# Optimization experiments

Hardware: AMD Instinct MI355X
Metric: run time of the kernel (lower is better)

The kernel has to match this reference:

```python
import jax, jax.numpy as jnp
import numpy as np
import math

B, D, OUT, K = 128, 128, 100000, 4096
T = 0.07
# NOTE: original code reads momentum as params[4], which is -1 (params = [K, T, -1, -1, -1, momentum]).
# We replicate this faithfully: effective momentum = -1.0.
MOMENTUM = -1.0


def setup_inputs() -> dict:
    key = jax.random.key(0)
    k1, k2, k3, k4, k5, k6, k7 = jax.random.split(key, 7)
    stdv = 1.0 / math.sqrt(D / 3)
    return {
        "z1": jax.random.normal(k1, (B, D), dtype=jnp.float32),
        "z2": jax.random.normal(k2, (B, D), dtype=jnp.float32),
        "z3": jax.random.normal(k3, (B, D), dtype=jnp.float32),
        "memory_z2": jax.random.uniform(k4, (OUT, D), dtype=jnp.float32, minval=-stdv, maxval=stdv),
        "memory_z3": jax.random.uniform(k5, (OUT, D), dtype=jnp.float32, minval=-stdv, maxval=stdv),
        "y": jax.random.randint(k6, (B,), 0, OUT, dtype=jnp.int32),
        "idx": jax.random.randint(k7, (B, K + 1), 0, OUT, dtype=jnp.int32),
    }


def _scores(memory, idx, z1, outputSize):
    # gather [B, K+1, D] rows, per-row dot with z1 -> [B, K+1]
    w = jax.lax.stop_gradient(memory)[idx]
    s = jnp.exp(jnp.einsum('bkd,bd->bk', w, z1) / T)[..., None]  # [B, K+1, 1]
    Z = jax.lax.stop_gradient(jnp.mean(s) * outputSize)  # Z_* set on first call
    return s / Z


def _update(memory, y, z):
    pos = memory[y] * MOMENTUM + z * (1.0 - MOMENTUM)  # [B, D]
    pos = pos / jnp.sqrt(jnp.sum(pos * pos, axis=1, keepdims=True))
    return memory.at[y].set(pos)


def reference(z1, z2, z3, memory_z2, memory_z3, y, idx):
    outputSize = memory_z2.shape[0]
    # mimic idx=None path: first column of idx is the positive index y
    idx = idx.at[:, 0].set(y)
    I_z12 = _scores(memory_z2, idx, z1, outputSize)
    I_z13 = _scores(memory_z3, idx, z1, outputSize)
    new_mem2 = _update(memory_z2, y, z2)
    new_mem3 = _update(memory_z3, y, z3)
    return (I_z12, I_z13, new_mem2, new_mem3)
```

## Files before the change

### kernel.cpp

```cpp
#include <hip/hip_runtime.h>

#define BB   128
#define DD   128
#define OUTN 100000
#define KP1  4097
#define TEMP 0.07f

#define NSB   8320
#define N1F4  3200000
#define NF4   6400000
#define CSTRIDE (NSB * 256)
#define SCORES (2 * BB * KP1)
#define NSCALE_BLK 4097

typedef float vfloat4 __attribute__((ext_vector_type(4)));

__global__ __launch_bounds__(256) void fused_kernel(
    const float* __restrict__ z1,
    const float* __restrict__ mem2,
    const float* __restrict__ mem3,
    const int*   __restrict__ y,
    const int*   __restrict__ idx,
    float* __restrict__ out,
    float* __restrict__ part)
{
    const int sb    = blockIdx.x;
    const int b     = sb & (BB - 1);
    const int chunk = sb >> 7;
    const int tid   = threadIdx.x;
    const int g     = tid & 7;
    const int grp   = tid >> 3;

    const float4* zz = (const float4*)(z1 + (size_t)b * DD + g * 16);
    const float4 z0 = zz[0], zv1 = zz[1], zv2 = zz[2], zv3 = zz[3];

    const int yb = y[b];

    float acc2 = 0.f, acc3 = 0.f;

    for (int it = 0; it < 2; ++it) {
        const int k = chunk * 64 + it * 32 + grp;
        const bool valid = (k < KP1);
        int j = 0;
        if (valid) j = (k == 0) ? yb : idx[b * KP1 + k];

        const float4* r2 = (const float4*)(mem2 + (size_t)j * DD + g * 16);
        const float4* r3 = (const float4*)(mem3 + (size_t)j * DD + g * 16);
        const float4 a0 = r2[0], a1 = r2[1], a2 = r2[2], a3 = r2[3];
        const float4 c0 = r3[0], c1 = r3[1], c2 = r3[2], c3 = r3[3];

        float d2 = a0.x*z0.x  + a0.y*z0.y  + a0.z*z0.z  + a0.w*z0.w
                 + a1.x*zv1.x + a1.y*zv1.y + a1.z*zv1.z + a1.w*zv1.w
                 + a2.x*zv2.x + a2.y*zv2.y + a2.z*zv2.z + a2.w*zv2.w
                 + a3.x*zv3.x + a3.y*zv3.y + a3.z*zv3.z + a3.w*zv3.w;
        float d3 = c0.x*z0.x  + c0.y*z0.y  + c0.z*z0.z  + c0.w*z0.w
                 + c1.x*zv1.x + c1.y*zv1.y + c1.z*zv1.z + c1.w*zv1.w
                 + c2.x*zv2.x + c2.y*zv2.y + c2.z*zv2.z + c2.w*zv2.w
                 + c3.x*zv3.x + c3.y*zv3.y + c3.z*zv3.z + c3.w*zv3.w;

        d2 += __shfl_xor(d2, 1);  d3 += __shfl_xor(d3, 1);
        d2 += __shfl_xor(d2, 2);  d3 += __shfl_xor(d3, 2);
        d2 += __shfl_xor(d2, 4);  d3 += __shfl_xor(d3, 4);

        if (valid && g == 0) {
            const float s2 = expf(d2 * (1.0f / TEMP));
            const float s3 = expf(d3 * (1.0f / TEMP));
            out[b * KP1 + k]            = s2;
            out[BB * KP1 + b * KP1 + k] = s3;
            acc2 += s2;
            acc3 += s3;
        }
    }

    {
        const vfloat4* m2f = (const vfloat4*)mem2;
        const vfloat4* m3f = (const vfloat4*)mem3;
        vfloat4* dstf = (vfloat4*)(out + SCORES);
        for (int i = sb * 256 + tid; i < NF4; i += CSTRIDE) {
            const vfloat4 v = (i < N1F4) ? m2f[i] : m3f[i - N1F4];
            __builtin_nontemporal_store(v, dstf + i);
        }
    }

    acc2 += __shfl_xor(acc2, 8);   acc3 += __shfl_xor(acc3, 8);
    acc2 += __shfl_xor(acc2, 16);  acc3 += __shfl_xor(acc3, 16);
    acc2 += __shfl_xor(acc2, 32);  acc3 += __shfl_xor(acc3, 32);

    __shared__ float w2s[4], w3s[4];
    const int wave = tid >> 6;
    const int lane = tid & 63;
    if (lane == 0) { w2s[wave] = acc2; w3s[wave] = acc3; }
    __syncthreads();
    if (tid == 0) {
        part[sb]       = w2s[0] + w2s[1] + w2s[2] + w2s[3];
        part[NSB + sb] = w3s[0] + w3s[1] + w3s[2] + w3s[3];
    }
}

__global__ __launch_bounds__(256) void finalize_kernel(
    const float* __restrict__ z2,
    const float* __restrict__ z3,
    const float* __restrict__ mem2,
    const float* __restrict__ mem3,
    const int*   __restrict__ y,
    float* __restrict__ out,
    const float* __restrict__ part)
{
    const int t = threadIdx.x;

    if (blockIdx.x < NSCALE_BLK) {
        float t2 = 0.f, t3 = 0.f;
        for (int i = t; i < NSB; i += 256) {
            t2 += part[i];
            t3 += part[NSB + i];
        }
        #pragma unroll
        for (int off = 32; off > 0; off >>= 1) {
            t2 += __shfl_xor(t2, off);
            t3 += __shfl_xor(t3, off);
        }
        __shared__ float r2[4], r3[4];
        if ((t & 63) == 0) { r2[t >> 6] = t2; r3[t >> 6] = t3; }
        __syncthreads();
        const float s2sum = r2[0] + r2[1] + r2[2] + r2[3];
        const float s3sum = r3[0] + r3[1] + r3[2] + r3[3];
        const float sc2 = (float)((double)(BB * KP1) / ((double)OUTN * (double)s2sum));
        const float sc3 = (float)((double)(BB * KP1) / ((double)OUTN * (double)s3sum));
        const int i = blockIdx.x * 256 + t;
        out[i] *= (i < BB * KP1) ? sc2 : sc3;
        return;
    }

    const int b  = blockIdx.x - NSCALE_BLK;
    const int yb = y[b];

    __shared__ int dup;
    if (t == 0) dup = 0;
    __syncthreads();
    if (t > b && t < BB && y[t] == yb) dup = 1;
    __syncthreads();
    if (dup) return;
    if (t >= 64) return;

    float* out2 = out + SCORES;
    float* out3 = out2 + OUTN * DD;

    const float2 m2 = *(const float2*)(mem2 + (size_t)yb * DD + 2 * t);
    const float2 m3 = *(const float2*)(mem3 + (size_t)yb * DD + 2 * t);
    const float2 a2 = *(const float2*)(z2 + b * DD + 2 * t);
    const float2 a3 = *(const float2*)(z3 + b * DD + 2 * t);

    float2 p2, p3;
    p2.x = 2.f * a2.x - m2.x;  p2.y = 2.f * a2.y - m2.y;
    p3.x = 2.f * a3.x - m3.x;  p3.y = 2.f * a3.y - m3.y;

    float ss2 = p2.x * p2.x + p2.y * p2.y;
    float ss3 = p3.x * p3.x + p3.y * p3.y;
    #pragma unroll
    for (int off = 32; off > 0; off >>= 1) {
        ss2 += __shfl_xor(ss2, off);
        ss3 += __shfl_xor(ss3, off);
    }
    const float inv2 = 1.f / sqrtf(ss2);
    const float inv3 = 1.f / sqrtf(ss3);

    float2 w2, w3;
    w2.x = p2.x * inv2;  w2.y = p2.y * inv2;
    w3.x = p3.x * inv3;  w3.y = p3.y * inv3;
    *(float2*)(out2 + (size_t)yb * DD + 2 * t) = w2;
    *(float2*)(out3 + (size_t)yb * DD + 2 * t) = w3;
}

extern "C" void kernel_launch(void* const* d_in, const int* in_sizes, int n_in,
                              void* d_out, int out_size, void* d_ws, size_t ws_size,
                              hipStream_t stream)
{
    const float* z1   = (const float*)d_in[0];
    const float* z2   = (const float*)d_in[1];
    const float* z3   = (const float*)d_in[2];
    const float* mem2 = (const float*)d_in[3];
    const float* mem3 = (const float*)d_in[4];
    const int*   y    = (const int*)d_in[5];
    const int*   idx  = (const int*)d_in[6];
    float*       out  = (float*)d_out;
    float*       part = (float*)d_ws;

    fused_kernel<<<NSB, 256, 0, stream>>>(z1, mem2, mem3, y, idx, out, part);

    finalize_kernel<<<NSCALE_BLK + BB, 256, 0, stream>>>(
        z2, z3, mem2, mem3, y, out, part);
}
```

Baseline: 280.0 us.

## Give each gather block four work items and reduce partial sums with atomics

The fused gather/dot kernel now launches a quarter as many blocks, and each block handles four (batch, chunk) work items. All index loads are hoisted ahead of the loop so more row gathers can be in flight per thread. Per-block partial sums are atomically added into 64 slots, which are zeroed by a memset before launch, so every scale block in the finalize kernel reads 128 floats instead of 16640. This adds an extra memset launch and atomic contention, and makes the float summation order nondeterministic.

```diff
diff --git a/kernel.cpp b/kernel.cpp
--- a/kernel.cpp
+++ b/kernel.cpp
@@ -7,9 +7,10 @@
 #define TEMP 0.07f
 
 #define NSB   8320
+#define NPB   2080
+#define ITERS 4
 #define N1F4  3200000
 #define NF4   6400000
-#define CSTRIDE (NSB * 256)
 #define SCORES (2 * BB * KP1)
 #define NSCALE_BLK 4097
 
@@ -24,51 +25,68 @@
     float* __restrict__ out,
     float* __restrict__ part)
 {
-    const int sb    = blockIdx.x;
-    const int b     = sb & (BB - 1);
-    const int chunk = sb >> 7;
-    const int tid   = threadIdx.x;
-    const int g     = tid & 7;
-    const int grp   = tid >> 3;
-
-    const float4* zz = (const float4*)(z1 + (size_t)b * DD + g * 16);
-    const float4 z0 = zz[0], zv1 = zz[1], zv2 = zz[2], zv3 = zz[3];
-
-    const int yb = y[b];
+    const int bid = blockIdx.x;
+    const int tid = threadIdx.x;
+    const int g   = tid & 7;
+    const int grp = tid >> 3;
+
+    int jj0[ITERS], jj1[ITERS];
+    #pragma unroll
+    for (int it = 0; it < ITERS; ++it) {
+        const int sb    = bid + it * NPB;
+        const int b     = sb & (BB - 1);
+        const int chunk = sb >> 7;
+        const int k0    = chunk * 64 + grp;
+        const int k1    = k0 + 32;
+        int j0 = 0, j1 = 0;
+        if (k0 < KP1) j0 = (k0 == 0) ? y[b] : idx[b * KP1 + k0];
+        if (k1 < KP1) j1 = idx[b * KP1 + k1];
+        jj0[it] = j0;  jj1[it] = j1;
+    }
 
     float acc2 = 0.f, acc3 = 0.f;
 
-    for (int it = 0; it < 2; ++it) {
-        const int k = chunk * 64 + it * 32 + grp;
-        const bool valid = (k < KP1);
-        int j = 0;
-        if (valid) j = (k == 0) ? yb : idx[b * KP1 + k];
-
-        const float4* r2 = (const float4*)(mem2 + (size_t)j * DD + g * 16);
-        const float4* r3 = (const float4*)(mem3 + (size_t)j * DD + g * 16);
-        const float4 a0 = r2[0], a1 = r2[1], a2 = r2[2], a3 = r2[3];
-        const float4 c0 = r3[0], c1 = r3[1], c2 = r3[2], c3 = r3[3];
-
-        float d2 = a0.x*z0.x  + a0.y*z0.y  + a0.z*z0.z  + a0.w*z0.w
-                 + a1.x*zv1.x + a1.y*zv1.y + a1.z*zv1.z + a1.w*zv1.w
-                 + a2.x*zv2.x + a2.y*zv2.y + a2.z*zv2.z + a2.w*zv2.w
-                 + a3.x*zv3.x + a3.y*zv3.y + a3.z*zv3.z + a3.w*zv3.w;
-        float d3 = c0.x*z0.x  + c0.y*z0.y  + c0.z*z0.z  + c0.w*z0.w
-                 + c1.x*zv1.x + c1.y*zv1.y + c1.z*zv1.z + c1.w*zv1.w
-                 + c2.x*zv2.x + c2.y*zv2.y + c2.z*zv2.z + c2.w*zv2.w
-                 + c3.x*zv3.x + c3.y*zv3.y + c3.z*zv3.z + c3.w*zv3.w;
-
-        d2 += __shfl_xor(d2, 1);  d3 += __shfl_xor(d3, 1);
-        d2 += __shfl_xor(d2, 2);  d3 += __shfl_xor(d3, 2);
-        d2 += __shfl_xor(d2, 4);  d3 += __shfl_xor(d3, 4);
-
-        if (valid && g == 0) {
-            const float s2 = expf(d2 * (1.0f / TEMP));
-            const float s3 = expf(d3 * (1.0f / TEMP));
-            out[b * KP1 + k]            = s2;
-            out[BB * KP1 + b * KP1 + k] = s3;
-            acc2 += s2;
-            acc3 += s3;
+    #pragma unroll
+    for (int it = 0; it < ITERS; ++it) {
+        const int sb    = bid + it * NPB;
+        const int b     = sb & (BB - 1);
+        const int chunk = sb >> 7;
+
+        const float4* zz = (const float4*)(z1 + (size_t)b * DD + g * 16);
+        const float4 z0 = zz[0], zv1 = zz[1], zv2 = zz[2], zv3 = zz[3];
+
+        #pragma unroll
+        for (int p = 0; p < 2; ++p) {
+            const int k     = chunk * 64 + p * 32 + grp;
+            const bool valid = (k < KP1);
+            const int j     = p ? jj1[it] : jj0[it];
+
+            const float4* r2 = (const float4*)(mem2 + (size_t)j * DD + g * 16);
+            const float4* r3 = (const float4*)(mem3 + (size_t)j * DD + g * 16);
+            const float4 a0 = r2[0], a1 = r2[1], a2 = r2[2], a3 = r2[3];
+            const float4 c0 = r3[0], c1 = r3[1], c2 = r3[2], c3 = r3[3];
+
+            float d2 = a0.x*z0.x  + a0.y*z0.y  + a0.z*z0.z  + a0.w*z0.w
+                     + a1.x*zv1.x + a1.y*zv1.y + a1.z*zv1.z + a1.w*zv1.w
+                     + a2.x*zv2.x + a2.y*zv2.y + a2.z*zv2.z + a2.w*zv2.w
+                     + a3.x*zv3.x + a3.y*zv3.y + a3.z*zv3.z + a3.w*zv3.w;
+            float d3 = c0.x*z0.x  + c0.y*z0.y  + c0.z*z0.z  + c0.w*z0.w
+                     + c1.x*zv1.x + c1.y*zv1.y + c1.z*zv1.z + c1.w*zv1.w
+                     + c2.x*zv2.x + c2.y*zv2.y + c2.z*zv2.z + c2.w*zv2.w
+                     + c3.x*zv3.x + c3.y*zv3.y + c3.z*zv3.z + c3.w*zv3.w;
+
+            d2 += __shfl_xor(d2, 1);  d3 += __shfl_xor(d3, 1);
+            d2 += __shfl_xor(d2, 2);  d3 += __shfl_xor(d3, 2);
+            d2 += __shfl_xor(d2, 4);  d3 += __shfl_xor(d3, 4);
+
+            if (valid && g == 0) {
+                const float s2 = expf(d2 * (1.0f / TEMP));
+                const float s3 = expf(d3 * (1.0f / TEMP));
+                out[b * KP1 + k]            = s2;
+                out[BB * KP1 + b * KP1 + k] = s3;
+                acc2 += s2;
+                acc3 += s3;
+            }
         }
     }
 
@@ -76,7 +94,7 @@
         const vfloat4* m2f = (const vfloat4*)mem2;
         const vfloat4* m3f = (const vfloat4*)mem3;
         vfloat4* dstf = (vfloat4*)(out + SCORES);
-        for (int i = sb * 256 + tid; i < NF4; i += CSTRIDE) {
+        for (int i = bid * 256 + tid; i < NF4; i += NPB * 256) {
             const vfloat4 v = (i < N1F4) ? m2f[i] : m3f[i - N1F4];
             __builtin_nontemporal_store(v, dstf + i);
         }
@@ -92,8 +110,11 @@
     if (lane == 0) { w2s[wave] = acc2; w3s[wave] = acc3; }
     __syncthreads();
     if (tid == 0) {
-        part[sb]       = w2s[0] + w2s[1] + w2s[2] + w2s[3];
-        part[NSB + sb] = w3s[0] + w3s[1] + w3s[2] + w3s[3];
+        const float t2 = w2s[0] + w2s[1] + w2s[2] + w2s[3];
+        const float t3 = w3s[0] + w3s[1] + w3s[2] + w3s[3];
+        const int slot = bid & 63;
+        atomicAdd(&part[slot],      t2);
+        atomicAdd(&part[64 + slot], t3);
     }
 }
 
@@ -109,25 +130,16 @@
     const int t = threadIdx.x;
 
     if (blockIdx.x < NSCALE_BLK) {
-        float t2 = 0.f, t3 = 0.f;
-        for (int i = t; i < NSB; i += 256) {
-            t2 += part[i];
-            t3 += part[NSB + i];
+        __shared__ float sc[2];
+        if (t == 0) {
+            float t2 = 0.f, t3 = 0.f;
+            for (int i = 0; i < 64; ++i) { t2 += part[i]; t3 += part[64 + i]; }
+            sc[0] = (float)((double)(BB * KP1) / ((double)OUTN * (double)t2));
+            sc[1] = (float)((double)(BB * KP1) / ((double)OUTN * (double)t3));
         }
-        #pragma unroll
-        for (int off = 32; off > 0; off >>= 1) {
-            t2 += __shfl_xor(t2, off);
-            t3 += __shfl_xor(t3, off);
-        }
-        __shared__ float r2[4], r3[4];
-        if ((t & 63) == 0) { r2[t >> 6] = t2; r3[t >> 6] = t3; }
         __syncthreads();
-        const float s2sum = r2[0] + r2[1] + r2[2] + r2[3];
-        const float s3sum = r3[0] + r3[1] + r3[2] + r3[3];
-        const float sc2 = (float)((double)(BB * KP1) / ((double)OUTN * (double)s2sum));
-        const float sc3 = (float)((double)(BB * KP1) / ((double)OUTN * (double)s3sum));
         const int i = blockIdx.x * 256 + t;
-        out[i] *= (i < BB * KP1) ? sc2 : sc3;
+        out[i] *= sc[(i < BB * KP1) ? 0 : 1];
         return;
     }
 
@@ -185,7 +197,9 @@
     float*       out  = (float*)d_out;
     float*       part = (float*)d_ws;
 
-    fused_kernel<<<NSB, 256, 0, stream>>>(z1, mem2, mem3, y, idx, out, part);
+    hipMemsetAsync(d_ws, 0, 128 * sizeof(float), stream);
+
+    fused_kernel<<<NPB, 256, 0, stream>>>(z1, mem2, mem3, y, idx, out, part);
 
     finalize_kernel<<<NSCALE_BLK + BB, 256, 0, stream>>>(
         z2, z3, mem2, mem3, y, out, part);
```

After: 275.7 us. No clear change (-1.5%).
